# Performance work log

Hardware: AMD Instinct MI355X
Metric: run time of the kernel (lower is better)

## Reference

```python
import jax, jax.numpy as jnp
import numpy as np

N_USERS = 100000
M_ITEMS = 200000
N_NODES = N_USERS + M_ITEMS
N_EDGES = 1200000
D = 64
N_LAYERS = 3
BATCH = 4096


def setup_inputs() -> dict:
    key = jax.random.key(0)
    ks = jax.random.split(key, 11)
    return {
        "users": jax.random.randint(ks[0], (BATCH,), 0, N_USERS),
        "items": jax.random.randint(ks[1], (BATCH,), 0, M_ITEMS),
        "rows": jax.random.randint(ks[2], (N_EDGES,), 0, N_NODES),
        "cols": jax.random.randint(ks[3], (N_EDGES,), 0, N_NODES),
        "vals": jax.random.uniform(ks[4], (N_EDGES,), dtype=jnp.float32),
        "user_emb": jax.random.normal(ks[5], (N_USERS, D), dtype=jnp.float32) * 0.1,
        "item_emb": jax.random.normal(ks[6], (M_ITEMS, D), dtype=jnp.float32) * 0.1,
        "W_gc": jax.random.normal(ks[7], (N_LAYERS, D, D), dtype=jnp.float32) * 0.1,
        "b_gc": jax.random.normal(ks[8], (N_LAYERS, D), dtype=jnp.float32) * 0.1,
        "W_bi": jax.random.normal(ks[9], (N_LAYERS, D, D), dtype=jnp.float32) * 0.1,
        "b_bi": jax.random.normal(ks[10], (N_LAYERS, D), dtype=jnp.float32) * 0.1,
    }


def _spmm(rows, cols, vals, x):
    # sparse.mm(Graph, x): out[r] = sum_e vals[e] * x[cols[e]] for rows[e]==r
    gathered = vals[:, None] * x[cols]  # [E, D]
    return jax.ops.segment_sum(gathered, rows, num_segments=N_NODES)


def _computer(rows, cols, vals, user_emb, item_emb, W_gc, b_gc, W_bi, b_bi):
    ego = jnp.concatenate([user_emb, item_emb], axis=0)  # [N, D]
    embs = [ego]
    for k in range(N_LAYERS):
        side = _spmm(rows, cols, vals, ego)
        sum_emb = side @ W_gc[k] + b_gc[k]
        bi_emb = (ego * side) @ W_bi[k] + b_bi[k]
        ego = jax.nn.leaky_relu(sum_emb + bi_emb, negative_slope=0.2)
        nrm = jnp.linalg.norm(ego, axis=1, keepdims=True)
        ego = ego / jnp.maximum(nrm, 1e-12)
        embs.append(ego)
    mean_emb = jnp.mean(jnp.stack(embs, axis=1), axis=1)  # [N, D]
    return mean_emb[:N_USERS], mean_emb[N_USERS:]


def reference(users, items, rows, cols, vals, user_emb, item_emb, W_gc, b_gc, W_bi, b_bi):
    all_users, all_items = _computer(rows, cols, vals, user_emb, item_emb, W_gc, b_gc, W_bi, b_bi)
    u = all_users[users]  # [B, D]
    i = all_items[items]  # [B, D]
    return jnp.sum(u * i, axis=1)  # [B]
```

## Files before the change

### kernel.cpp

```cpp
#include <hip/hip_runtime.h>
#include <hip/hip_bf16.h>

#define N_USERS 100000
#define M_ITEMS 200000
#define N_NODES 300000
#define N_EDGES 1200000
#define BATCH   4096
#define NB      ((N_NODES + 255) / 256)
#define CHUNK   5
#define EPT4    (N_EDGES / 4)
#define EGRID4  ((EPT4 + 255) / 256)

typedef __attribute__((ext_vector_type(8))) short short8;
typedef __attribute__((ext_vector_type(4))) float floatx4;

static __device__ __forceinline__ float b2f(__hip_bfloat16 x) { return __bfloat162float(x); }

static __device__ __forceinline__ short f2bs(float f) {
    union { __hip_bfloat16 h; short s; } u;
    u.h = __float2bfloat16(f);
    return u.s;
}
static __device__ __forceinline__ float us2f(unsigned int us) {
    return __uint_as_float(us << 16);
}

static __device__ __forceinline__ float loadf(const void* p, int i, int isbf) {
    if (isbf) return b2f(((const __hip_bfloat16*)p)[i]);
    return ((const float*)p)[i];
}

static __device__ __forceinline__ int sniff_dev(const void* vals) {
    const unsigned short* v16 = (const unsigned short*)vals;
    int c = 0;
#pragma unroll
    for (int i = 0; i < 16; ++i) {
        unsigned int ub = (v16[2 * i] >> 8) & 0xFF;
        if (ub >= 0x3A && ub <= 0x3F) ++c;
    }
    return (c >= 12) ? 1 : 0;
}

static __device__ __forceinline__ void unpack8(float* o, uint4 e) {
    unsigned int w[4] = {e.x, e.y, e.z, e.w};
#pragma unroll
    for (int j = 0; j < 8; ++j) o[j] = us2f((w[j >> 1] >> ((j & 1) * 16)) & 0xFFFFu);
}

static __device__ __forceinline__ const unsigned short* bfsrc(
    const void* ue, const void* ie, int n64) {
    return (n64 < N_USERS * 64)
        ? (const unsigned short*)ue + (size_t)(unsigned)n64
        : (const unsigned short*)ie + (size_t)(unsigned)(n64 - N_USERS * 64);
}
static __device__ __forceinline__ const float* fsrc(
    const void* ue, const void* ie, int n64) {
    return (n64 < N_USERS * 64)
        ? (const float*)ue + (size_t)(unsigned)n64
        : (const float*)ie + (size_t)(unsigned)(n64 - N_USERS * 64);
}

static __device__ __forceinline__ void gather16o(
    float* o0, float* o1, const unsigned short* ego,
    const void* ue, const void* ie, int n64, int quad, int isbf, int use_src) {
    if (!use_src) {
        const unsigned short* p = ego + (size_t)(unsigned)n64 + quad * 8;
        unpack8(o0, *(const uint4*)p);
        unpack8(o1, *(const uint4*)(p + 32));
    } else if (isbf) {
        const unsigned short* p = bfsrc(ue, ie, n64) + quad * 8;
        unpack8(o0, *(const uint4*)p);
        unpack8(o1, *(const uint4*)(p + 32));
    } else {
        const float* p = fsrc(ue, ie, n64) + quad * 8;
        float4 a = *(const float4*)p;
        float4 b = *(const float4*)(p + 4);
        float4 c = *(const float4*)(p + 32);
        float4 d = *(const float4*)(p + 36);
        o0[0]=a.x; o0[1]=a.y; o0[2]=a.z; o0[3]=a.w; o0[4]=b.x; o0[5]=b.y; o0[6]=b.z; o0[7]=b.w;
        o1[0]=c.x; o1[1]=c.y; o1[2]=c.z; o1[3]=c.w; o1[4]=d.x; o1[5]=d.y; o1[6]=d.z; o1[7]=d.w;
    }
}

static __device__ __forceinline__ void fma8x2(
    float* s0, float* s1, float v, uint4 a, uint4 b) {
    float t0[8], t1[8];
    unpack8(t0, a);
    unpack8(t1, b);
#pragma unroll
    for (int j = 0; j < 8; ++j) {
        s0[j] = fmaf(v, t0[j], s0[j]);
        s1[j] = fmaf(v, t1[j], s1[j]);
    }
}

static __device__ __forceinline__ void fma8x2f(
    float* s0, float* s1, float v, float4 a, float4 b, float4 c, float4 d) {
    s0[0]=fmaf(v,a.x,s0[0]); s0[1]=fmaf(v,a.y,s0[1]); s0[2]=fmaf(v,a.z,s0[2]); s0[3]=fmaf(v,a.w,s0[3]);
    s0[4]=fmaf(v,b.x,s0[4]); s0[5]=fmaf(v,b.y,s0[5]); s0[6]=fmaf(v,b.z,s0[6]); s0[7]=fmaf(v,b.w,s0[7]);
    s1[0]=fmaf(v,c.x,s1[0]); s1[1]=fmaf(v,c.y,s1[1]); s1[2]=fmaf(v,c.z,s1[2]); s1[3]=fmaf(v,c.w,s1[3]);
    s1[4]=fmaf(v,d.x,s1[4]); s1[5]=fmaf(v,d.y,s1[5]); s1[6]=fmaf(v,d.z,s1[6]); s1[7]=fmaf(v,d.w,s1[7]);
}

__global__ __launch_bounds__(256) void setup_kernel(
    const void* __restrict__ Wg, const void* __restrict__ bg,
    const void* __restrict__ Wb, const void* __restrict__ bb,
    const void* __restrict__ vals,
    const int* __restrict__ users, const int* __restrict__ items,
    unsigned short* __restrict__ WT, float* __restrict__ sb,
    unsigned char* __restrict__ f1, unsigned char* __restrict__ f2,
    unsigned char* __restrict__ f3) {
    if (blockIdx.x < 12) {
        int isbf = __builtin_amdgcn_readfirstlane(sniff_dev(vals));
        int t = blockIdx.x * 256 + threadIdx.x;
        if (t < 3072) {
            int lane = t & 63, h = (t >> 6) & 1, ct = (t >> 7) & 3, w = (t >> 9) & 1, k = t >> 10;
            int m = lane & 15, quad = lane >> 4;
            const void* Wsrc = w ? Wb : Wg;
#pragma unroll
            for (int j = 0; j < 8; ++j) {
                int kk = h * 32 + quad * 8 + j;
                WT[(size_t)(k * 1024 + w * 512 + ct * 128 + h * 64 + lane) * 8 + j] =
                    (unsigned short)f2bs(loadf(Wsrc, k * 4096 + kk * 64 + ct * 16 + m, isbf));
            }
        }
        if (t < 192) sb[t] = loadf(bg, t, isbf) + loadf(bb, t, isbf);
    } else {
        int i = (blockIdx.x - 12) * 256 + threadIdx.x;
        int n = -1;
        if (i < BATCH) n = users[i];
        else if (i < 2 * BATCH) n = N_USERS + items[i - BATCH];
        if (n >= 0) { f1[n] = 1; f2[n] = 1; f3[n] = 1; }
    }
}

__global__ __launch_bounds__(256) void prop_kernel(
    const int4* __restrict__ rows4, const int4* __restrict__ cols4,
    const unsigned char* __restrict__ src, unsigned char* __restrict__ dst) {
    int t = blockIdx.x * 256 + threadIdx.x;
    if (t < EPT4) {
        int4 r = rows4[t];
        int4 c = cols4[t];
        if (src[r.x]) dst[c.x] = 1;
        if (src[r.y]) dst[c.y] = 1;
        if (src[r.z]) dst[c.z] = 1;
        if (src[r.w]) dst[c.w] = 1;
    }
}

__global__ __launch_bounds__(256) void count_rank_kernel(
    const int4* __restrict__ rows4, const unsigned char* __restrict__ flag1,
    int* __restrict__ off, uint2* __restrict__ rank) {
    int t = blockIdx.x * 256 + threadIdx.x;
    if (t < EPT4) {
        int4 r = rows4[t];
        unsigned int k0 = 0xFFFFu, k1 = 0xFFFFu, k2 = 0xFFFFu, k3 = 0xFFFFu;
        if (flag1[r.x]) k0 = (unsigned int)atomicAdd(&off[r.x + 1], 1);
        if (flag1[r.y]) k1 = (unsigned int)atomicAdd(&off[r.y + 1], 1);
        if (flag1[r.z]) k2 = (unsigned int)atomicAdd(&off[r.z + 1], 1);
        if (flag1[r.w]) k3 = (unsigned int)atomicAdd(&off[r.w + 1], 1);
        rank[t] = make_uint2((k0 & 0xFFFFu) | (k1 << 16), (k2 & 0xFFFFu) | (k3 << 16));
    }
}

static __device__ __forceinline__ int deg_class(int d) {
    return d >= 16 ? 0 : d >= 8 ? 1 : d >= 4 ? 2 : 3;
}

__global__ __launch_bounds__(256) void scanA_kernel(
    const int* __restrict__ off, const unsigned char* __restrict__ flags,
    int* __restrict__ bsum, int* __restrict__ bcnt, unsigned char* __restrict__ cls) {
    __shared__ int s[256];
    __shared__ int w[4];
    int t = threadIdx.x;
    int n = blockIdx.x * 256 + t;
    bool ir = (n < N_NODES);
    int deg = ir ? off[n + 1] : 0;
    s[t] = deg;
    __syncthreads();
    for (int o = 128; o >= 1; o >>= 1) {
        if (t < o) s[t] += s[t + o];
        __syncthreads();
    }
    if (t == 0) bsum[blockIdx.x] = s[0];
    int c = deg_class(deg);
    if (ir) cls[n] = (unsigned char)c;
    int lane = t & 63;
    int wid  = t >> 6;
#pragma unroll
    for (int L = 0; L < 3; ++L) {
        bool fl = ir && flags[L * N_NODES + n];
#pragma unroll
        for (int cc = 0; cc < 4; ++cc) {
            unsigned long long mask = __ballot(fl && (c == cc));
            if (lane == 0) w[wid] = __popcll(mask);
            __syncthreads();
            if (t == 0) bcnt[(L * 4 + cc) * NB + blockIdx.x] = w[0] + w[1] + w[2] + w[3];
            __syncthreads();
        }
    }
}

__global__ __launch_bounds__(256) void scanB_kernel(
    int* __restrict__ bsum, int* __restrict__ bcnt, int* __restrict__ cnts) {
    __shared__ int s[256];
    int t = threadIdx.x;
    {
        int base = t * CHUNK, loc = 0;
        for (int j = 0; j < CHUNK; ++j) { int i = base + j; if (i < NB) loc += bsum[i]; }
        s[t] = loc;
        __syncthreads();
        for (int o = 1; o < 256; o <<= 1) {
            int add = (t >= o) ? s[t - o] : 0;
            __syncthreads();
            s[t] += add;
            __syncthreads();
        }
        int run = (t == 0) ? 0 : s[t - 1];
        for (int j = 0; j < CHUNK; ++j) {
            int i = base + j;
            if (i < NB) { int tmp = bsum[i]; bsum[i] = run; run += tmp; }
        }
        __syncthreads();
    }
    for (int L = 0; L < 3; ++L) {
        int levelRun = 0;
        for (int c = 0; c < 4; ++c) {
            int v = L * 4 + c;
            int base = t * CHUNK;
            int loc = 0;
            for (int j = 0; j < CHUNK; ++j) { int i = base + j; if (i < NB) loc += bcnt[v * NB + i]; }
            s[t] = loc;
            __syncthreads();
            for (int o = 1; o < 256; o <<= 1) {
                int add = (t >= o) ? s[t - o] : 0;
                __syncthreads();
                s[t] += add;
                __syncthreads();
            }
            int run = ((t == 0) ? 0 : s[t - 1]) + levelRun;
            int total = s[255];
            for (int j = 0; j < CHUNK; ++j) {
                int i = base + j;
                if (i < NB) { int tmp = bcnt[v * NB + i]; bcnt[v * NB + i] = run; run += tmp; }
            }
            levelRun += total;
            __syncthreads();
        }
        if (t == 0) cnts[L] = levelRun;
    }
}

__global__ __launch_bounds__(256) void scanC_kernel(
    int* __restrict__ off, const int* __restrict__ bsum,
    const unsigned char* __restrict__ flags, const unsigned char* __restrict__ cls,
    const int* __restrict__ bcnt, int* __restrict__ lists, int* __restrict__ map3) {
    __shared__ int s[256];
    __shared__ int wsum[4];
    int t = threadIdx.x;
    int n = blockIdx.x * 256 + t;
    bool ir = (n < N_NODES);
    s[t] = ir ? off[n + 1] : 0;
    __syncthreads();
    for (int o = 1; o < 256; o <<= 1) {
        int add = (t >= o) ? s[t - o] : 0;
        __syncthreads();
        s[t] += add;
        __syncthreads();
    }
    if (ir) off[n + 1] = s[t] + bsum[blockIdx.x];
    int c = ir ? (int)cls[n] : 3;
    int lane = t & 63;
    int wid  = t >> 6;
#pragma unroll
    for (int L = 0; L < 3; ++L) {
        bool fl = ir && flags[L * N_NODES + n];
#pragma unroll
        for (int cc = 0; cc < 4; ++cc) {
            bool f = fl && (c == cc);
            unsigned long long mask = __ballot(f);
            if (lane == 0) wsum[wid] = __popcll(mask);
            __syncthreads();
            int base = bcnt[(L * 4 + cc) * NB + blockIdx.x];
            for (int i = 0; i < wid; ++i) base += wsum[i];
            if (f) {
                int pos = base + __popcll(mask & ((1ull << lane) - 1ull));
                lists[L * N_NODES + pos] = n;
                if (L == 2) map3[n] = pos + 1;
            }
            __syncthreads();
        }
    }
}

__global__ __launch_bounds__(256) void fill_kernel(
    const int4* __restrict__ rows4, const int4* __restrict__ cols4,
    const void* __restrict__ vals, const int* __restrict__ off,
    const uint2* __restrict__ rank, int2* __restrict__ epack) {
    int isbf = __builtin_amdgcn_readfirstlane(sniff_dev(vals));
    int t = blockIdx.x * 256 + threadIdx.x;
    if (t < EPT4) {
        int4 r = rows4[t];
        int4 c = cols4[t];
        uint2 kk = rank[t];
        unsigned int k0 = kk.x & 0xFFFFu, k1 = kk.x >> 16;
        unsigned int k2 = kk.y & 0xFFFFu, k3 = kk.y >> 16;
        int e = t * 4;
        if (k0 != 0xFFFFu)
            epack[off[r.x] + (int)k0] = make_int2(c.x << 6, __float_as_int(loadf(vals, e, isbf)));
        if (k1 != 0xFFFFu)
            epack[off[r.y] + (int)k1] = make_int2(c.y << 6, __float_as_int(loadf(vals, e + 1, isbf)));
        if (k2 != 0xFFFFu)
            epack[off[r.z] + (int)k2] = make_int2(c.z << 6, __float_as_int(loadf(vals, e + 2, isbf)));
        if (k3 != 0xFFFFu)
            epack[off[r.w] + (int)k3] = make_int2(c.w << 6, __float_as_int(loadf(vals, e + 3, isbf)));
    }
}

template<int USE_SRC>
__global__ __launch_bounds__(256) void fused_layer_kernel(
    const int* __restrict__ off, const int2* __restrict__ epack,
    const unsigned short* __restrict__ ego_in,
    const void* __restrict__ ue, const void* __restrict__ ie,
    const void* __restrict__ vals,
    const unsigned short* __restrict__ WT, const float* __restrict__ sb,
    int klayer, unsigned short* __restrict__ ego_out,
    const int* __restrict__ list, const int* __restrict__ cntp,
    const int* __restrict__ map3, float* __restrict__ acc) {
    const int isbf = USE_SRC ? __builtin_amdgcn_readfirstlane(sniff_dev(vals)) : 0;
    const int cnt  = __builtin_amdgcn_readfirstlane(cntp[0]);
    const int ntile = (cnt + 15) >> 4;
    const int lane = threadIdx.x & 63;
    const int m    = lane & 15;
    const int quad = lane >> 4;

    const unsigned short* wt = WT + (size_t)klayer * 8192;
    float bv[4];
#pragma unroll
    for (int ct = 0; ct < 4; ++ct) bv[ct] = sb[klayer * 64 + ct * 16 + m];

    const int wv = blockIdx.x * 4 + (threadIdx.x >> 6);
    const int nw = gridDim.x * 4;
    for (int tile = wv; tile < ntile; tile += nw) {
        const int idx = tile * 16 + m;
        const int row = list[idx < cnt ? idx : cnt - 1];
        const int start = off[row];
        const int end   = off[row + 1];

        float s0[8] = {0,0,0,0,0,0,0,0};
        float s1[8] = {0,0,0,0,0,0,0,0};
        int e = start;
        if (!USE_SRC) {
            const unsigned short* eb = ego_in + quad * 8;
            for (; e + 4 <= end; e += 4) {
                int2 c0 = epack[e], c1 = epack[e + 1], c2 = epack[e + 2], c3 = epack[e + 3];
                const unsigned short* q0 = eb + (size_t)(unsigned)c0.x;
                const unsigned short* q1 = eb + (size_t)(unsigned)c1.x;
                const unsigned short* q2 = eb + (size_t)(unsigned)c2.x;
                const unsigned short* q3 = eb + (size_t)(unsigned)c3.x;
                uint4 a0 = *(const uint4*)q0, b0 = *(const uint4*)(q0 + 32);
                uint4 a1 = *(const uint4*)q1, b1 = *(const uint4*)(q1 + 32);
                uint4 a2 = *(const uint4*)q2, b2 = *(const uint4*)(q2 + 32);
                uint4 a3 = *(const uint4*)q3, b3 = *(const uint4*)(q3 + 32);
                fma8x2(s0, s1, __int_as_float(c0.y), a0, b0);
                fma8x2(s0, s1, __int_as_float(c1.y), a1, b1);
                fma8x2(s0, s1, __int_as_float(c2.y), a2, b2);
                fma8x2(s0, s1, __int_as_float(c3.y), a3, b3);
            }
        } else if (isbf) {
            for (; e + 4 <= end; e += 4) {
                int2 c0 = epack[e], c1 = epack[e + 1], c2 = epack[e + 2], c3 = epack[e + 3];
                const unsigned short* q0 = bfsrc(ue, ie, c0.x) + quad * 8;
                const unsigned short* q1 = bfsrc(ue, ie, c1.x) + quad * 8;
                const unsigned short* q2 = bfsrc(ue, ie, c2.x) + quad * 8;
                const unsigned short* q3 = bfsrc(ue, ie, c3.x) + quad * 8;
                uint4 a0 = *(const uint4*)q0, b0 = *(const uint4*)(q0 + 32);
                uint4 a1 = *(const uint4*)q1, b1 = *(const uint4*)(q1 + 32);
                uint4 a2 = *(const uint4*)q2, b2 = *(const uint4*)(q2 + 32);
                uint4 a3 = *(const uint4*)q3, b3 = *(const uint4*)(q3 + 32);
                fma8x2(s0, s1, __int_as_float(c0.y), a0, b0);
                fma8x2(s0, s1, __int_as_float(c1.y), a1, b1);
                fma8x2(s0, s1, __int_as_float(c2.y), a2, b2);
                fma8x2(s0, s1, __int_as_float(c3.y), a3, b3);
            }
        } else {
            for (; e + 3 <= end; e += 3) {
                int2 c0 = epack[e], c1 = epack[e + 1], c2 = epack[e + 2];
                const float* p0 = fsrc(ue, ie, c0.x) + quad * 8;
                const float* p1 = fsrc(ue, ie, c1.x) + quad * 8;
                const float* p2 = fsrc(ue, ie, c2.x) + quad * 8;
                float4 x0 = *(const float4*)p0, y0 = *(const float4*)(p0 + 4);
                float4 z0 = *(const float4*)(p0 + 32), w0 = *(const float4*)(p0 + 36);
                float4 x1 = *(const float4*)p1, y1 = *(const float4*)(p1 + 4);
                float4 z1 = *(const float4*)(p1 + 32), w1 = *(const float4*)(p1 + 36);
                float4 x2 = *(const float4*)p2, y2 = *(const float4*)(p2 + 4);
                float4 z2 = *(const float4*)(p2 + 32), w2 = *(const float4*)(p2 + 36);
                fma8x2f(s0, s1, __int_as_float(c0.y), x0, y0, z0, w0);
                fma8x2f(s0, s1, __int_as_float(c1.y), x1, y1, z1, w1);
                fma8x2f(s0, s1, __int_as_float(c2.y), x2, y2, z2, w2);
            }
        }
        for (; e < end; ++e) {
            int2 cv = epack[e];
            float v = __int_as_float(cv.y);
            float t0[8], t1[8];
            gather16o(t0, t1, ego_in, ue, ie, cv.x, quad, isbf, USE_SRC);
#pragma unroll
            for (int j = 0; j < 8; ++j) {
                s0[j] = fmaf(v, t0[j], s0[j]);
                s1[j] = fmaf(v, t1[j], s1[j]);
            }
        }

        float eg0[8], eg1[8];
        gather16o(eg0, eg1, ego_in, ue, ie, row << 6, quad, isbf, USE_SRC);

        short8 As0, As1, Ap0, Ap1;
#pragma unroll
        for (int j = 0; j < 8; ++j) {
            As0[j] = f2bs(s0[j]);
            As1[j] = f2bs(s1[j]);
            Ap0[j] = f2bs(eg0[j] * s0[j]);
            Ap1[j] = f2bs(eg1[j] * s1[j]);
        }

        float v[4][4];
        float ssq[4] = {0.f, 0.f, 0.f, 0.f};
#pragma unroll
        for (int ct = 0; ct < 4; ++ct) {
            short8 Bg0 = *(const short8*)(wt + (size_t)((ct * 2 + 0) * 64 + lane) * 8);
            short8 Bg1 = *(const short8*)(wt + (size_t)((ct * 2 + 1) * 64 + lane) * 8);
            short8 Bb0 = *(const short8*)(wt + (size_t)(512 + (ct * 2 + 0) * 64 + lane) * 8);
            short8 Bb1 = *(const short8*)(wt + (size_t)(512 + (ct * 2 + 1) * 64 + lane) * 8);
            floatx4 a = {0.f, 0.f, 0.f, 0.f};
            a = __builtin_amdgcn_mfma_f32_16x16x32_bf16(As0, Bg0, a, 0, 0, 0);
            a = __builtin_amdgcn_mfma_f32_16x16x32_bf16(As1, Bg1, a, 0, 0, 0);
            a = __builtin_amdgcn_mfma_f32_16x16x32_bf16(Ap0, Bb0, a, 0, 0, 0);
            a = __builtin_amdgcn_mfma_f32_16x16x32_bf16(Ap1, Bb1, a, 0, 0, 0);
#pragma unroll
            for (int r = 0; r < 4; ++r) {
                float x = a[r] + bv[ct];
                x = x > 0.f ? x : 0.2f * x;
                v[ct][r] = x;
                ssq[r] += x * x;
            }
        }
#pragma unroll
        for (int o = 1; o < 16; o <<= 1)
#pragma unroll
            for (int r = 0; r < 4; ++r) ssq[r] += __shfl_xor(ssq[r], o, 64);
#pragma unroll
        for (int r = 0; r < 4; ++r) {
            int idx_w = tile * 16 + quad * 4 + r;
            if (idx_w < cnt) {
                float sc = 1.0f / fmaxf(sqrtf(ssq[r]), 1e-12f);
                int rw = list[idx_w];
                int c3 = map3[rw];
#pragma unroll
                for (int ct = 0; ct < 4; ++ct)
                    ego_out[(size_t)rw * 64 + ct * 16 + m] = (unsigned short)f2bs(v[ct][r] * sc);
                if (c3 > 0) {
                    float* ap = acc + (size_t)(c3 - 1) * 64 + m;
#pragma unroll
                    for (int ct = 0; ct < 4; ++ct) ap[ct * 16] += v[ct][r] * sc;
                }
            }
        }
    }
}

__global__ __launch_bounds__(256) void dot_kernel(
    const int* __restrict__ users, const int* __restrict__ items,
    const float* __restrict__ acc, const int* __restrict__ map3,
    const void* __restrict__ ue, const void* __restrict__ ie,
    void* __restrict__ out, const void* __restrict__ vals) {
    int isbf = __builtin_amdgcn_readfirstlane(sniff_dev(vals));
    int gid = blockIdx.x * 256 + threadIdx.x;
    int b = gid >> 6;
    int lane = gid & 63;
    int un = __builtin_amdgcn_readfirstlane(users[b]);
    int in_ = __builtin_amdgcn_readfirstlane(items[b]);
    int cu = __builtin_amdgcn_readfirstlane(map3[un]);
    int ci = __builtin_amdgcn_readfirstlane(map3[N_USERS + in_]);
    float u = (cu > 0 ? acc[(size_t)(cu - 1) * 64 + lane] : 0.f) + loadf(ue, un * 64 + lane, isbf);
    float v = (ci > 0 ? acc[(size_t)(ci - 1) * 64 + lane] : 0.f) + loadf(ie, in_ * 64 + lane, isbf);
    float pr = u * v;
#pragma unroll
    for (int o = 32; o >= 1; o >>= 1) pr += __shfl_xor(pr, o, 64);
    if (lane == 0) {
        float r = pr * 0.0625f;
        if (isbf) ((__hip_bfloat16*)out)[b] = __float2bfloat16(r);
        else      ((float*)out)[b] = r;
    }
}

static inline size_t align16(size_t x) { return (x + 15) & ~(size_t)15; }

extern "C" void kernel_launch(void* const* d_in, const int* in_sizes, int n_in,
                              void* d_out, int out_size, void* d_ws, size_t ws_size,
                              hipStream_t stream) {
    const int* users = (const int*)d_in[0];
    const int* items = (const int*)d_in[1];
    const int* rows  = (const int*)d_in[2];
    const int* cols  = (const int*)d_in[3];
    const void* vals     = d_in[4];
    const void* user_emb = d_in[5];
    const void* item_emb = d_in[6];
    const void* W_gc     = d_in[7];
    const void* b_gc     = d_in[8];
    const void* W_bi     = d_in[9];
    const void* b_bi     = d_in[10];

    const size_t egoB   = (size_t)N_NODES * 64 * sizeof(short);
    const size_t packB  = (size_t)N_EDGES * sizeof(int2);
    const size_t rankB  = (size_t)EPT4 * sizeof(uint2);
    const size_t bsumB  = (size_t)NB * sizeof(int);
    const size_t bcntB  = (size_t)12 * NB * sizeof(int);
    const size_t clsB   = (size_t)N_NODES;
    const size_t wtB    = (size_t)3 * 1024 * 8 * sizeof(short);
    const size_t sbB    = (size_t)192 * sizeof(float);
    const size_t accB   = (size_t)2 * BATCH * 64 * sizeof(float);
    const size_t offB   = (size_t)(N_NODES + 1) * sizeof(int);
    const size_t cntsB  = (size_t)8 * sizeof(int);
    const size_t map3B  = (size_t)N_NODES * sizeof(int);
    const size_t flagsB = (size_t)3 * N_NODES;

    char* ws = (char*)d_ws;
    size_t o = 0;
    unsigned short* egoA  = (unsigned short*)(ws + o); o += egoB;
    unsigned short* egoB2 = (unsigned short*)(ws + o); o += egoB;
    int2*  epack  = (int2*)(ws + o);  o += packB;
    uint2* rank   = (uint2*)(ws + o); o += rankB;
    int*   bsum   = (int*)(ws + o);   o += bsumB;
    int*   bcnt   = (int*)(ws + o);   o += bcntB;
    unsigned char* cls = (unsigned char*)(ws + o); o += clsB;
    o = align16(o);
    unsigned short* WT = (unsigned short*)(ws + o); o += wtB;
    float* sb     = (float*)(ws + o); o += sbB;
    o = align16(o);
    float* acc    = (float*)(ws + o);
    int*   off    = (int*)((char*)acc + accB);
    int*   cnts   = (int*)((char*)off + offB);
    int*   map3   = (int*)((char*)cnts + cntsB);
    unsigned char* flags = (unsigned char*)((char*)map3 + map3B);
    const size_t zeroB = accB + offB + cntsB + map3B + flagsB;
    unsigned char* flagL[3] = {flags, flags + N_NODES, flags + 2 * N_NODES};
    int* lists = (int*)(flags + flagsB);
    int* listL[3] = {lists, lists + N_NODES, lists + 2 * N_NODES};

    hipMemsetAsync(acc, 0, zeroB, stream);

    setup_kernel<<<44, 256, 0, stream>>>(W_gc, b_gc, W_bi, b_bi, vals, users, items,
                                         WT, sb, flagL[0], flagL[1], flagL[2]);

    prop_kernel<<<EGRID4, 256, 0, stream>>>((const int4*)rows, (const int4*)cols, flagL[2], flagL[1]);
    prop_kernel<<<EGRID4, 256, 0, stream>>>((const int4*)rows, (const int4*)cols, flagL[1], flagL[0]);

    count_rank_kernel<<<EGRID4, 256, 0, stream>>>((const int4*)rows, flagL[0], off, rank);

    scanA_kernel<<<NB, 256, 0, stream>>>(off, flags, bsum, bcnt, cls);
    scanB_kernel<<<1, 256, 0, stream>>>(bsum, bcnt, cnts);
    scanC_kernel<<<NB, 256, 0, stream>>>(off, bsum, flags, cls, bcnt, lists, map3);

    fill_kernel<<<EGRID4, 256, 0, stream>>>((const int4*)rows, (const int4*)cols, vals, off, rank, epack);

    fused_layer_kernel<1><<<2048, 256, 0, stream>>>(off, epack, egoA, user_emb, item_emb,
                                                    vals, WT, sb, 0, egoA,
                                                    listL[0], cnts + 0, map3, acc);
    fused_layer_kernel<0><<<2048, 256, 0, stream>>>(off, epack, egoA, user_emb, item_emb,
                                                    vals, WT, sb, 1, egoB2,
                                                    listL[1], cnts + 1, map3, acc);
    fused_layer_kernel<0><<<2048, 256, 0, stream>>>(off, epack, egoB2, user_emb, item_emb,
                                                    vals, WT, sb, 2, egoA,
                                                    listL[2], cnts + 2, map3, acc);
    dot_kernel<<<(BATCH * 64) / 256, 256, 0, stream>>>(users, items, acc, map3,
                                                       user_emb, item_emb, d_out, vals);
}
```

Before: 305.3 us.

## Build full CSR unconditionally and derive frontier flags from CSR instead of edge passes

Drops the two full edge-list propagation passes and the flag-gated counting. The new code builds a complete CSR for all rows, merges the first frontier propagation into the fill pass, and computes the second frontier by walking the CSR adjacency of flagged nodes only. This removes one full pass over 1.2M edges and the dependence of counting on flags. In exchange, every edge now takes an atomic and an epack write, not just edges of needed rows, and the scan is split into more kernel launches.

New measurement: 348.0 us. 14.0% more time.

```diff
diff --git a/kernel.cpp b/kernel.cpp
--- a/kernel.cpp
+++ b/kernel.cpp
@@ -134,57 +134,127 @@
     }
 }
 
-__global__ __launch_bounds__(256) void prop_kernel(
+__global__ __launch_bounds__(256) void count_all_kernel(
+    const int4* __restrict__ rows4, int* __restrict__ off, uint2* __restrict__ rank) {
+    int t = blockIdx.x * 256 + threadIdx.x;
+    if (t < EPT4) {
+        int4 r = rows4[t];
+        unsigned int k0 = (unsigned int)atomicAdd(&off[r.x + 1], 1);
+        unsigned int k1 = (unsigned int)atomicAdd(&off[r.y + 1], 1);
+        unsigned int k2 = (unsigned int)atomicAdd(&off[r.z + 1], 1);
+        unsigned int k3 = (unsigned int)atomicAdd(&off[r.w + 1], 1);
+        rank[t] = make_uint2((k0 & 0xFFFFu) | (k1 << 16), (k2 & 0xFFFFu) | (k3 << 16));
+    }
+}
+
+static __device__ __forceinline__ int deg_class(int d) {
+    return d >= 16 ? 0 : d >= 8 ? 1 : d >= 4 ? 2 : 3;
+}
+
+__global__ __launch_bounds__(256) void scanOffA_kernel(
+    const int* __restrict__ A, int* __restrict__ bsum) {
+    __shared__ int s[256];
+    int t = threadIdx.x;
+    int i = blockIdx.x * 256 + t;
+    s[t] = (i < N_NODES) ? A[i] : 0;
+    __syncthreads();
+    for (int o = 128; o >= 1; o >>= 1) {
+        if (t < o) s[t] += s[t + o];
+        __syncthreads();
+    }
+    if (t == 0) bsum[blockIdx.x] = s[0];
+}
+
+__global__ __launch_bounds__(256) void scanOffB_kernel(int* __restrict__ bsum) {
+    __shared__ int s[256];
+    int t = threadIdx.x;
+    int base = t * CHUNK;
+    int loc = 0;
+    for (int j = 0; j < CHUNK; ++j) { int i = base + j; if (i < NB) loc += bsum[i]; }
+    s[t] = loc;
+    __syncthreads();
+    for (int o = 1; o < 256; o <<= 1) {
+        int add = (t >= o) ? s[t - o] : 0;
+        __syncthreads();
+        s[t] += add;
+        __syncthreads();
+    }
+    int run = (t == 0) ? 0 : s[t - 1];
+    for (int j = 0; j < CHUNK; ++j) {
+        int i = base + j;
+        if (i < NB) { int tmp = bsum[i]; bsum[i] = run; run += tmp; }
+    }
+}
+
+__global__ __launch_bounds__(256) void scanOffC_kernel(
+    int* __restrict__ A, const int* __restrict__ bsum, unsigned char* __restrict__ cls) {
+    __shared__ int s[256];
+    int t = threadIdx.x;
+    int i = blockIdx.x * 256 + t;
+    int deg = (i < N_NODES) ? A[i] : 0;
+    s[t] = deg;
+    __syncthreads();
+    for (int o = 1; o < 256; o <<= 1) {
+        int add = (t >= o) ? s[t - o] : 0;
+        __syncthreads();
+        s[t] += add;
+        __syncthreads();
+    }
+    if (i < N_NODES) {
+        A[i] = s[t] + bsum[blockIdx.x];
+        cls[i] = (unsigned char)deg_class(deg);
+    }
+}
+
+__global__ __launch_bounds__(256) void fill_all_kernel(
     const int4* __restrict__ rows4, const int4* __restrict__ cols4,
-    const unsigned char* __restrict__ src, unsigned char* __restrict__ dst) {
+    const void* __restrict__ vals, const int* __restrict__ off,
+    const uint2* __restrict__ rank, int2* __restrict__ epack,
+    const unsigned char* __restrict__ f3, unsigned char* __restrict__ f2) {
+    int isbf = __builtin_amdgcn_readfirstlane(sniff_dev(vals));
     int t = blockIdx.x * 256 + threadIdx.x;
     if (t < EPT4) {
         int4 r = rows4[t];
         int4 c = cols4[t];
-        if (src[r.x]) dst[c.x] = 1;
-        if (src[r.y]) dst[c.y] = 1;
-        if (src[r.z]) dst[c.z] = 1;
-        if (src[r.w]) dst[c.w] = 1;
-    }
-}
-
-__global__ __launch_bounds__(256) void count_rank_kernel(
-    const int4* __restrict__ rows4, const unsigned char* __restrict__ flag1,
-    int* __restrict__ off, uint2* __restrict__ rank) {
-    int t = blockIdx.x * 256 + threadIdx.x;
-    if (t < EPT4) {
-        int4 r = rows4[t];
-        unsigned int k0 = 0xFFFFu, k1 = 0xFFFFu, k2 = 0xFFFFu, k3 = 0xFFFFu;
-        if (flag1[r.x]) k0 = (unsigned int)atomicAdd(&off[r.x + 1], 1);
-        if (flag1[r.y]) k1 = (unsigned int)atomicAdd(&off[r.y + 1], 1);
-        if (flag1[r.z]) k2 = (unsigned int)atomicAdd(&off[r.z + 1], 1);
-        if (flag1[r.w]) k3 = (unsigned int)atomicAdd(&off[r.w + 1], 1);
-        rank[t] = make_uint2((k0 & 0xFFFFu) | (k1 << 16), (k2 & 0xFFFFu) | (k3 << 16));
-    }
-}
-
-static __device__ __forceinline__ int deg_class(int d) {
-    return d >= 16 ? 0 : d >= 8 ? 1 : d >= 4 ? 2 : 3;
-}
-
-__global__ __launch_bounds__(256) void scanA_kernel(
-    const int* __restrict__ off, const unsigned char* __restrict__ flags,
-    int* __restrict__ bsum, int* __restrict__ bcnt, unsigned char* __restrict__ cls) {
-    __shared__ int s[256];
+        uint2 kk = rank[t];
+        float v0, v1, v2, v3;
+        if (isbf) {
+            ushort4 vv = ((const ushort4*)vals)[t];
+            v0 = us2f(vv.x); v1 = us2f(vv.y); v2 = us2f(vv.z); v3 = us2f(vv.w);
+        } else {
+            float4 vv = ((const float4*)vals)[t];
+            v0 = vv.x; v1 = vv.y; v2 = vv.z; v3 = vv.w;
+        }
+        epack[off[r.x] + (int)(kk.x & 0xFFFFu)] = make_int2(c.x << 6, __float_as_int(v0));
+        epack[off[r.y] + (int)(kk.x >> 16)]     = make_int2(c.y << 6, __float_as_int(v1));
+        epack[off[r.z] + (int)(kk.y & 0xFFFFu)] = make_int2(c.z << 6, __float_as_int(v2));
+        epack[off[r.w] + (int)(kk.y >> 16)]     = make_int2(c.w << 6, __float_as_int(v3));
+        if (f3[r.x]) f2[c.x] = 1;
+        if (f3[r.y]) f2[c.y] = 1;
+        if (f3[r.z]) f2[c.z] = 1;
+        if (f3[r.w]) f2[c.w] = 1;
+    }
+}
+
+__global__ __launch_bounds__(256) void expand2_kernel(
+    const unsigned char* __restrict__ f2, const int* __restrict__ off,
+    const int2* __restrict__ epack, unsigned char* __restrict__ f1) {
+    int n = blockIdx.x * 256 + threadIdx.x;
+    if (n < N_NODES && f2[n]) {
+        f1[n] = 1;
+        int e0 = off[n], e1 = off[n + 1];
+        for (int e = e0; e < e1; ++e) f1[(unsigned)epack[e].x >> 6] = 1;
+    }
+}
+
+__global__ __launch_bounds__(256) void scanListA_kernel(
+    const unsigned char* __restrict__ flags, const unsigned char* __restrict__ cls,
+    int* __restrict__ bcnt) {
     __shared__ int w[4];
     int t = threadIdx.x;
     int n = blockIdx.x * 256 + t;
     bool ir = (n < N_NODES);
-    int deg = ir ? off[n + 1] : 0;
-    s[t] = deg;
-    __syncthreads();
-    for (int o = 128; o >= 1; o >>= 1) {
-        if (t < o) s[t] += s[t + o];
-        __syncthreads();
-    }
-    if (t == 0) bsum[blockIdx.x] = s[0];
-    int c = deg_class(deg);
-    if (ir) cls[n] = (unsigned char)c;
+    int c = ir ? (int)cls[n] : 3;
     int lane = t & 63;
     int wid  = t >> 6;
 #pragma unroll
@@ -201,28 +271,10 @@
     }
 }
 
-__global__ __launch_bounds__(256) void scanB_kernel(
-    int* __restrict__ bsum, int* __restrict__ bcnt, int* __restrict__ cnts) {
+__global__ __launch_bounds__(256) void scanListB_kernel(
+    int* __restrict__ bcnt, int* __restrict__ cnts) {
     __shared__ int s[256];
     int t = threadIdx.x;
-    {
-        int base = t * CHUNK, loc = 0;
-        for (int j = 0; j < CHUNK; ++j) { int i = base + j; if (i < NB) loc += bsum[i]; }
-        s[t] = loc;
-        __syncthreads();
-        for (int o = 1; o < 256; o <<= 1) {
-            int add = (t >= o) ? s[t - o] : 0;
-            __syncthreads();
-            s[t] += add;
-            __syncthreads();
-        }
-        int run = (t == 0) ? 0 : s[t - 1];
-        for (int j = 0; j < CHUNK; ++j) {
-            int i = base + j;
-            if (i < NB) { int tmp = bsum[i]; bsum[i] = run; run += tmp; }
-        }
-        __syncthreads();
-    }
     for (int L = 0; L < 3; ++L) {
         int levelRun = 0;
         for (int c = 0; c < 4; ++c) {
@@ -251,24 +303,13 @@
     }
 }
 
-__global__ __launch_bounds__(256) void scanC_kernel(
-    int* __restrict__ off, const int* __restrict__ bsum,
+__global__ __launch_bounds__(256) void scanListC_kernel(
     const unsigned char* __restrict__ flags, const unsigned char* __restrict__ cls,
     const int* __restrict__ bcnt, int* __restrict__ lists, int* __restrict__ map3) {
-    __shared__ int s[256];
     __shared__ int wsum[4];
     int t = threadIdx.x;
     int n = blockIdx.x * 256 + t;
     bool ir = (n < N_NODES);
-    s[t] = ir ? off[n + 1] : 0;
-    __syncthreads();
-    for (int o = 1; o < 256; o <<= 1) {
-        int add = (t >= o) ? s[t - o] : 0;
-        __syncthreads();
-        s[t] += add;
-        __syncthreads();
-    }
-    if (ir) off[n + 1] = s[t] + bsum[blockIdx.x];
     int c = ir ? (int)cls[n] : 3;
     int lane = t & 63;
     int wid  = t >> 6;
@@ -290,30 +331,6 @@
             }
             __syncthreads();
         }
-    }
-}
-
-__global__ __launch_bounds__(256) void fill_kernel(
-    const int4* __restrict__ rows4, const int4* __restrict__ cols4,
-    const void* __restrict__ vals, const int* __restrict__ off,
-    const uint2* __restrict__ rank, int2* __restrict__ epack) {
-    int isbf = __builtin_amdgcn_readfirstlane(sniff_dev(vals));
-    int t = blockIdx.x * 256 + threadIdx.x;
-    if (t < EPT4) {
-        int4 r = rows4[t];
-        int4 c = cols4[t];
-        uint2 kk = rank[t];
-        unsigned int k0 = kk.x & 0xFFFFu, k1 = kk.x >> 16;
-        unsigned int k2 = kk.y & 0xFFFFu, k3 = kk.y >> 16;
-        int e = t * 4;
-        if (k0 != 0xFFFFu)
-            epack[off[r.x] + (int)k0] = make_int2(c.x << 6, __float_as_int(loadf(vals, e, isbf)));
-        if (k1 != 0xFFFFu)
-            epack[off[r.y] + (int)k1] = make_int2(c.y << 6, __float_as_int(loadf(vals, e + 1, isbf)));
-        if (k2 != 0xFFFFu)
-            epack[off[r.z] + (int)k2] = make_int2(c.z << 6, __float_as_int(loadf(vals, e + 2, isbf)));
-        if (k3 != 0xFFFFu)
-            epack[off[r.w] + (int)k3] = make_int2(c.w << 6, __float_as_int(loadf(vals, e + 3, isbf)));
     }
 }
 
@@ -553,16 +570,20 @@
     setup_kernel<<<44, 256, 0, stream>>>(W_gc, b_gc, W_bi, b_bi, vals, users, items,
                                          WT, sb, flagL[0], flagL[1], flagL[2]);
 
-    prop_kernel<<<EGRID4, 256, 0, stream>>>((const int4*)rows, (const int4*)cols, flagL[2], flagL[1]);
-    prop_kernel<<<EGRID4, 256, 0, stream>>>((const int4*)rows, (const int4*)cols, flagL[1], flagL[0]);
-
-    count_rank_kernel<<<EGRID4, 256, 0, stream>>>((const int4*)rows, flagL[0], off, rank);
-
-    scanA_kernel<<<NB, 256, 0, stream>>>(off, flags, bsum, bcnt, cls);
-    scanB_kernel<<<1, 256, 0, stream>>>(bsum, bcnt, cnts);
-    scanC_kernel<<<NB, 256, 0, stream>>>(off, bsum, flags, cls, bcnt, lists, map3);
-
-    fill_kernel<<<EGRID4, 256, 0, stream>>>((const int4*)rows, (const int4*)cols, vals, off, rank, epack);
+    count_all_kernel<<<EGRID4, 256, 0, stream>>>((const int4*)rows, off, rank);
+
+    scanOffA_kernel<<<NB, 256, 0, stream>>>(off + 1, bsum);
+    scanOffB_kernel<<<1, 256, 0, stream>>>(bsum);
+    scanOffC_kernel<<<NB, 256, 0, stream>>>(off + 1, bsum, cls);
+
+    fill_all_kernel<<<EGRID4, 256, 0, stream>>>((const int4*)rows, (const int4*)cols, vals,
+                                                off, rank, epack, flagL[2], flagL[1]);
+
+    expand2_kernel<<<NB, 256, 0, stream>>>(flagL[1], off, epack, flagL[0]);
+
+    scanListA_kernel<<<NB, 256, 0, stream>>>(flags, cls, bcnt);
+    scanListB_kernel<<<1, 256, 0, stream>>>(bcnt, cnts);
+    scanListC_kernel<<<NB, 256, 0, stream>>>(flags, cls, bcnt, lists, map3);
 
     fused_layer_kernel<1><<<2048, 256, 0, stream>>>(off, epack, egoA, user_emb, item_emb,
                                                     vals, WT, sb, 0, egoA,
```
